# Kernel optimization log

Measured on AMD Instinct MI355X. Metric: run time of the kernel, lower is better.

The kernel has to match this reference:

```python
import jax, jax.numpy as jnp
import numpy as np

B, C, E = 2, 1024, 1024
H = 16            # n_heads as declared (used as per-group feature dim due to module's reshape)
HD = E // H       # 64 — the axis actually batched over in attention


def setup_inputs() -> dict:
    key = jax.random.key(0)
    ks = jax.random.split(key, 5)
    scale = 0.02
    return {
        "x": jax.random.normal(ks[0], (B, C, E), dtype=jnp.float32),
        "W_q": jax.random.normal(ks[1], (E, E), dtype=jnp.float32) * scale,
        "W_k": jax.random.normal(ks[2], (E, E), dtype=jnp.float32) * scale,
        "W_v": jax.random.normal(ks[3], (E, E), dtype=jnp.float32) * scale,
        "W_o": jax.random.normal(ks[4], (E, E), dtype=jnp.float32) * scale,
    }


def reference(x, W_q, W_k, W_v, W_o):
    # nn.Linear: y = x @ W.T  (bias=False)
    def proj_split(W):
        y = jnp.einsum('bce,de->bcd', x, W)              # [B,C,E]
        # view(B, C, HD, H).transpose(1,2) -> [B, HD, C, H]  (faithful to source layout)
        return y.reshape(B, C, HD, H).transpose(0, 2, 1, 3)

    Q = proj_split(W_q)
    K = proj_split(W_k)
    V = proj_split(W_v)

    scale = 1.0 / jnp.sqrt(jnp.asarray(H, dtype=x.dtype))  # sqrt of last dim (= n_heads here)
    scores = jnp.einsum('bdqh,bdkh->bdqk', Q, K) * scale    # [B, HD, C, C]
    weights = jax.nn.softmax(scores, axis=-1)
    out = jnp.einsum('bdqk,bdkh->bdqh', weights, V)         # [B, HD, C, H]
    out = out.transpose(0, 2, 1, 3).reshape(B, C, E)        # [B, C, E]
    out = jnp.einsum('bce,de->bcd', out, W_o)
    return out  # dropout p=0.0 / eval mode: identity
```

## Files before the change

kernel.cpp:

```cpp
#include <hip/hip_runtime.h>
#include <stdint.h>
#include <math.h>


typedef __bf16   bf16x8 __attribute__((ext_vector_type(8)));
typedef float    f32x4  __attribute__((ext_vector_type(4)));

__device__ __forceinline__ unsigned short f2bf(float f) {
    unsigned int u = __float_as_uint(f);
    u += 0x7FFFu + ((u >> 16) & 1u);
    return (unsigned short)(u >> 16);
}

__device__ __forceinline__ unsigned int cvtpk(float lo, float hi) {
    unsigned int r;
    asm("v_cvt_pk_bf16_f32 %0, %1, %2" : "=v"(r) : "v"(lo), "v"(hi));
    return r;
}

__device__ __forceinline__ void gl16(const unsigned short* g, unsigned short* l) {
    __builtin_amdgcn_global_load_lds(
        (const __attribute__((address_space(1))) unsigned int*)g,
        (__attribute__((address_space(3))) unsigned int*)l, 16, 0, 0);
}

__global__ __launch_bounds__(256) void cast_to_bf16(
    const float* __restrict__ x,
    const float* __restrict__ w0, const float* __restrict__ w1,
    const float* __restrict__ w2, const float* __restrict__ w3,
    unsigned short* __restrict__ xb,
    unsigned short* __restrict__ b0, unsigned short* __restrict__ b1,
    unsigned short* __restrict__ b2, unsigned short* __restrict__ b3)
{
    const int z = blockIdx.y;
    const float* src;
    unsigned short* dst;
    size_t off = 0;
    float sc = 1.f;
    if (z < 2)       { src = x;  dst = xb; off = (size_t)z << 20; }
    else if (z == 2) { src = w0; dst = b0; sc = 0.36067376022224085f; }
    else if (z == 3) { src = w1; dst = b1; }
    else if (z == 4) { src = w2; dst = b2; }
    else             { src = w3; dst = b3; }
    const size_t i = off + ((size_t)blockIdx.x * 256 + threadIdx.x) * 4;
    const float4 v = *(const float4*)(src + i);
    *(ushort4*)(dst + i) = make_ushort4(f2bf(v.x * sc), f2bf(v.y * sc),
                                        f2bf(v.z * sc), f2bf(v.w * sc));
}

__global__ __launch_bounds__(256) void gemm128_bt_mfma(
    const unsigned short* __restrict__ A,
    const unsigned short* __restrict__ B0, const unsigned short* __restrict__ B1,
    const unsigned short* __restrict__ B2,
    unsigned short* __restrict__ C0, unsigned short* __restrict__ C1,
    unsigned short* __restrict__ C2,
    int M, int N, int K)
{
    const unsigned short* Bm = (blockIdx.z == 0) ? B0 : (blockIdx.z == 1) ? B1 : B2;
    unsigned short* Cm       = (blockIdx.z == 0) ? C0 : (blockIdx.z == 1) ? C1 : C2;

    __shared__ __align__(16) unsigned short As[2][128 * 32];
    __shared__ __align__(16) unsigned short Bs[2][128 * 32];

    const int t    = threadIdx.x;
    const int lane = t & 63;
    const int w    = t >> 6;
    const int m0   = blockIdx.y * 128;
    const int n0   = blockIdx.x * 128;
    const int wm   = (w & 1) * 64;
    const int wn   = (w >> 1) * 64;

    const int r0 = t >> 2;
    const int c0 = (t & 3) * 8;
    const unsigned short* Apa = A  + (size_t)(m0 + r0) * K + c0;
    const unsigned short* Apb = Apa + (size_t)64 * K;
    const unsigned short* Bpa = Bm + (size_t)(n0 + r0) * K + c0;
    const unsigned short* Bpb = Bpa + (size_t)64 * K;
    unsigned short* lA0 = &As[0][w * 512];
    unsigned short* lA1 = &As[0][2048 + w * 512];
    unsigned short* lB0 = &Bs[0][w * 512];
    unsigned short* lB1 = &Bs[0][2048 + w * 512];
    const int bufStr = 128 * 32;

    f32x4 acc[4][4];
#pragma unroll
    for (int i = 0; i < 4; ++i)
#pragma unroll
        for (int j = 0; j < 4; ++j) acc[i][j] = (f32x4){0.f, 0.f, 0.f, 0.f};

    const int fm = lane & 15;
    const int kg = lane >> 4;

    gl16(Apa, lA0);
    gl16(Apb, lA1);
    gl16(Bpa, lB0);
    gl16(Bpb, lB1);

    int cur = 0;
    for (int k0 = 0; k0 < K; k0 += 32) {
        __syncthreads();

        if (k0 + 32 < K) {
            const int nb = (cur ^ 1);
            gl16(Apa + k0 + 32, lA0 + nb * bufStr);
            gl16(Apb + k0 + 32, lA1 + nb * bufStr);
            gl16(Bpa + k0 + 32, lB0 + nb * bufStr);
            gl16(Bpb + k0 + 32, lB1 + nb * bufStr);
        }

        const unsigned short* Ab = &As[cur][0];
        const unsigned short* Bb = &Bs[cur][0];
        bf16x8 af[4], bfr[4];
#pragma unroll
        for (int im = 0; im < 4; ++im)
            af[im] = *(const bf16x8*)&Ab[(wm + im * 16 + fm) * 32 + kg * 8];
#pragma unroll
        for (int in = 0; in < 4; ++in)
            bfr[in] = *(const bf16x8*)&Bb[(wn + in * 16 + fm) * 32 + kg * 8];
#pragma unroll
        for (int im = 0; im < 4; ++im)
#pragma unroll
            for (int in = 0; in < 4; ++in)
                acc[im][in] = __builtin_amdgcn_mfma_f32_16x16x32_bf16(
                    af[im], bfr[in], acc[im][in], 0, 0, 0);

        cur ^= 1;
    }

#pragma unroll
    for (int im = 0; im < 4; ++im) {
#pragma unroll
        for (int in = 0; in < 4; ++in) {
            const int row = m0 + wm + im * 16 + kg * 4;
            const int col = n0 + wn + in * 16 + fm;
#pragma unroll
            for (int r = 0; r < 4; ++r)
                Cm[(size_t)(row + r) * N + col] = f2bf(acc[im][in][r]);
        }
    }
}

__global__ __launch_bounds__(256) void gemm_bt_mfma(
    const unsigned short* __restrict__ A,
    const unsigned short* __restrict__ B0, const unsigned short* __restrict__ B1,
    const unsigned short* __restrict__ B2,
    void* __restrict__ C0, void* __restrict__ C1, void* __restrict__ C2,
    int M, int N, int K, int bf16out)
{
    const unsigned short* Bm = (blockIdx.z == 0) ? B0 : (blockIdx.z == 1) ? B1 : B2;
    void* Cm                 = (blockIdx.z == 0) ? C0 : (blockIdx.z == 1) ? C1 : C2;

    __shared__ __align__(16) unsigned short As[2][64 * 32];
    __shared__ __align__(16) unsigned short Bs[2][128 * 32];

    const int t    = threadIdx.x;
    const int lane = t & 63;
    const int w    = t >> 6;
    const int m0   = blockIdx.y * 64;
    const int n0   = blockIdx.x * 128;
    const int wm   = (w & 1) * 32;
    const int wn   = (w >> 1) * 64;

    const int r0 = t >> 2;
    const int c0 = (t & 3) * 8;
    const unsigned short* Apa = A  + (size_t)(m0 + r0) * K + c0;
    const unsigned short* Bpa = Bm + (size_t)(n0 + r0) * K + c0;
    const unsigned short* Bpb = Bm + (size_t)(n0 + r0 + 64) * K + c0;
    unsigned short* ldsA  = &As[0][w * 512];
    unsigned short* ldsB0 = &Bs[0][w * 512];
    unsigned short* ldsB1 = &Bs[0][2048 + w * 512];
    const int bufStrA = 64 * 32;
    const int bufStrB = 128 * 32;

    f32x4 acc[2][4];
#pragma unroll
    for (int i = 0; i < 2; ++i)
#pragma unroll
        for (int j = 0; j < 4; ++j) acc[i][j] = (f32x4){0.f, 0.f, 0.f, 0.f};

    const int fm = lane & 15;
    const int kg = lane >> 4;

    gl16(Apa, ldsA);
    gl16(Bpa, ldsB0);
    gl16(Bpb, ldsB1);

    int cur = 0;
    for (int k0 = 0; k0 < K; k0 += 32) {
        __syncthreads();

        if (k0 + 32 < K) {
            const int nb = (cur ^ 1);
            gl16(Apa + k0 + 32, ldsA  + nb * bufStrA);
            gl16(Bpa + k0 + 32, ldsB0 + nb * bufStrB);
            gl16(Bpb + k0 + 32, ldsB1 + nb * bufStrB);
        }

        const unsigned short* Ab = &As[cur][0];
        const unsigned short* Bb = &Bs[cur][0];
        bf16x8 af[2], bfr[4];
#pragma unroll
        for (int im = 0; im < 2; ++im)
            af[im] = *(const bf16x8*)&Ab[(wm + im * 16 + fm) * 32 + kg * 8];
#pragma unroll
        for (int in = 0; in < 4; ++in)
            bfr[in] = *(const bf16x8*)&Bb[(wn + in * 16 + fm) * 32 + kg * 8];
#pragma unroll
        for (int im = 0; im < 2; ++im)
#pragma unroll
            for (int in = 0; in < 4; ++in)
                acc[im][in] = __builtin_amdgcn_mfma_f32_16x16x32_bf16(
                    af[im], bfr[in], acc[im][in], 0, 0, 0);

        cur ^= 1;
    }

#pragma unroll
    for (int im = 0; im < 2; ++im) {
#pragma unroll
        for (int in = 0; in < 4; ++in) {
            const int row = m0 + wm + im * 16 + kg * 4;
            const int col = n0 + wn + in * 16 + fm;
            if (bf16out) {
                unsigned short* cp = (unsigned short*)Cm;
#pragma unroll
                for (int r = 0; r < 4; ++r)
                    cp[(size_t)(row + r) * N + col] = f2bf(acc[im][in][r]);
            } else {
                float* cp = (float*)Cm;
#pragma unroll
                for (int r = 0; r < 4; ++r)
                    cp[(size_t)(row + r) * N + col] = acc[im][in][r];
            }
        }
    }
}

#define VSTRW 40
#define PSTRW 32

__global__ __launch_bounds__(256, 4) void attn_mfma(
    const unsigned short* __restrict__ Qb, const unsigned short* __restrict__ Kb,
    const unsigned short* __restrict__ Vb, unsigned short* __restrict__ Ob)
{
    __shared__ __align__(16) unsigned char smem[37888];

    const int t    = threadIdx.x;
    const int lane = t & 63;
    const int wv   = t >> 6;
    const int fm   = lane & 15;
    const int kg   = lane >> 4;
    const int bh   = blockIdx.y;
    const size_t base = ((size_t)(bh >> 6) << 20) + (size_t)(bh & 63) * 16;
    const int q0 = blockIdx.x * 128;
    const int wk = wv * 32;

    unsigned short* VsT = (unsigned short*)(smem + wv * 1280);
    unsigned short* Ps  = (unsigned short*)(smem + 5120 + wv * 8192);
    float*          Red = (float*)smem;

    union { uint4 u; bf16x8 h; } zz; zz.u = make_uint4(0, 0, 0, 0);
    bf16x8 aq[8];
#pragma unroll
    for (int m = 0; m < 8; ++m) {
        if (kg < 2)
            aq[m] = *(const bf16x8*)(Qb + base +
                     (size_t)(q0 + m * 16 + fm) * 1024 + kg * 8);
        else
            aq[m] = zz.h;
    }

    f32x4 oacc[8];
    float lp[8];
#pragma unroll
    for (int m = 0; m < 8; ++m) {
        oacc[m] = (f32x4){0.f, 0.f, 0.f, 0.f};
        lp[m] = 0.f;
    }

    for (int kt = 0; kt < 1024; kt += 128) {
        {
            const int key = lane >> 1, half = lane & 1;
            const uint4 v = *(const uint4*)(Vb + base +
                             (size_t)(kt + wk + key) * 1024 + half * 8);
            const unsigned short* pv = (const unsigned short*)&v;
#pragma unroll
            for (int d = 0; d < 8; ++d)
                VsT[(half * 8 + d) * VSTRW + key] = pv[d];
        }

        bf16x8 bk0 = zz.h, bk1 = zz.h;
        if (kg < 2) {
            bk0 = *(const bf16x8*)(Kb + base +
                   (size_t)(kt + wk + fm) * 1024 + kg * 8);
            bk1 = *(const bf16x8*)(Kb + base +
                   (size_t)(kt + wk + 16 + fm) * 1024 + kg * 8);
        }

#pragma unroll
        for (int m = 0; m < 8; ++m) {
            f32x4 s0 = __builtin_amdgcn_mfma_f32_16x16x32_bf16(
                bk0, aq[m], (f32x4){0.f, 0.f, 0.f, 0.f}, 0, 0, 0);
            f32x4 s1 = __builtin_amdgcn_mfma_f32_16x16x32_bf16(
                bk1, aq[m], (f32x4){0.f, 0.f, 0.f, 0.f}, 0, 0, 0);
            const float p0 = __builtin_amdgcn_exp2f(s0[0]);
            const float p1 = __builtin_amdgcn_exp2f(s0[1]);
            const float p2 = __builtin_amdgcn_exp2f(s0[2]);
            const float p3 = __builtin_amdgcn_exp2f(s0[3]);
            const float p4 = __builtin_amdgcn_exp2f(s1[0]);
            const float p5 = __builtin_amdgcn_exp2f(s1[1]);
            const float p6 = __builtin_amdgcn_exp2f(s1[2]);
            const float p7 = __builtin_amdgcn_exp2f(s1[3]);
            lp[m] += ((p0 + p1) + (p2 + p3)) + ((p4 + p5) + (p6 + p7));
            unsigned short* prow = Ps + (m * 16 + fm) * PSTRW;
            *(uint2*)&prow[kg * 4]      = make_uint2(cvtpk(p0, p1), cvtpk(p2, p3));
            *(uint2*)&prow[16 + kg * 4] = make_uint2(cvtpk(p4, p5), cvtpk(p6, p7));
        }

        const bf16x8 bv = *(const bf16x8*)&VsT[fm * VSTRW + kg * 8];
#pragma unroll
        for (int m = 0; m < 8; ++m) {
            const bf16x8 ap = *(const bf16x8*)&Ps[(m * 16 + fm) * PSTRW + kg * 8];
            oacc[m] = __builtin_amdgcn_mfma_f32_16x16x32_bf16(ap, bv, oacc[m], 0, 0, 0);
        }
    }

#pragma unroll
    for (int m = 0; m < 8; ++m) {
        lp[m] += __shfl_xor(lp[m], 16, 64);
        lp[m] += __shfl_xor(lp[m], 32, 64);
    }

    __syncthreads();
#pragma unroll
    for (int m = 0; m < 8; ++m) {
#pragma unroll
        for (int r = 0; r < 4; ++r)
            Red[((wv * 128) + m * 16 + kg * 4 + r) * 17 + fm] = oacc[m][r];
        if (kg == 0)
            Red[((wv * 128) + m * 16 + fm) * 17 + 16] = lp[m];
    }
    __syncthreads();

#pragma unroll
    for (int mp = 0; mp < 2; ++mp) {
#pragma unroll
        for (int r = 0; r < 4; ++r) {
            const int q = wv * 32 + mp * 16 + kg * 4 + r;
            const float o = Red[q * 17 + fm]         + Red[(128 + q) * 17 + fm] +
                            Red[(256 + q) * 17 + fm] + Red[(384 + q) * 17 + fm];
            const float l = Red[q * 17 + 16]         + Red[(128 + q) * 17 + 16] +
                            Red[(256 + q) * 17 + 16] + Red[(384 + q) * 17 + 16];
            Ob[base + (size_t)(q0 + q) * 1024 + fm] = f2bf(o / l);
        }
    }
}

extern "C" void kernel_launch(void* const* d_in, const int* in_sizes, int n_in,
                              void* d_out, int out_size, void* d_ws, size_t ws_size,
                              hipStream_t stream) {
    const float* x  = (const float*)d_in[0];
    const float* Wq = (const float*)d_in[1];
    const float* Wk = (const float*)d_in[2];
    const float* Wv = (const float*)d_in[3];
    const float* Wo = (const float*)d_in[4];
    float* out = (float*)d_out;

    const int M = 2048, N = 1024, Kd = 1024;
    const size_t MEG = 1048576;
    unsigned short* ws = (unsigned short*)d_ws;
    unsigned short* xb  = ws;
    unsigned short* Wqb = ws + 2 * MEG;
    unsigned short* Wkb = ws + 3 * MEG;
    unsigned short* Wvb = ws + 4 * MEG;
    unsigned short* Wob = ws + 5 * MEG;
    unsigned short* Qb  = ws + 6 * MEG;
    unsigned short* Kb  = ws + 8 * MEG;
    unsigned short* Vb  = ws + 10 * MEG;
    unsigned short* Ob  = ws + 12 * MEG;

    dim3 gc(1024, 6, 1);
    cast_to_bf16<<<gc, 256, 0, stream>>>(x, Wq, Wk, Wv, Wo, xb, Wqb, Wkb, Wvb, Wob);

    dim3 g1(N / 128, M / 128, 3);
    gemm128_bt_mfma<<<g1, 256, 0, stream>>>(xb, Wqb, Wkb, Wvb, Qb, Kb, Vb, M, N, Kd);

    dim3 g2(8, 128, 1);
    attn_mfma<<<g2, 256, 0, stream>>>(Qb, Kb, Vb, Ob);

    dim3 g3(N / 128, M / 64, 1);
    gemm_bt_mfma<<<g3, 256, 0, stream>>>(Ob, Wob, Wob, Wob, out, out, out, M, N, Kd, 0);
}
```

Baseline: 162.5 us.

## Keep P in registers by permuting V layout, stage K through LDS

Removes the LDS round-trip for the softmax probabilities. P values are packed straight into the MFMA A-operand, and V is stored transposed with a permuted key column order so it matches the register layout of the score accumulator. K is now loaded cooperatively into LDS with coalesced 16-byte loads instead of per-lane global reads. This cuts LDS write/read traffic and shared memory size, but relies on the permutation being correct, and still has no barrier between LDS store and load within each wave.

After: 143.8 us. -11.5%, faster.

```diff
diff --git a/kernel.cpp b/kernel.cpp
--- a/kernel.cpp
+++ b/kernel.cpp
@@ -10,12 +10,6 @@
     unsigned int u = __float_as_uint(f);
     u += 0x7FFFu + ((u >> 16) & 1u);
     return (unsigned short)(u >> 16);
-}
-
-__device__ __forceinline__ unsigned int cvtpk(float lo, float hi) {
-    unsigned int r;
-    asm("v_cvt_pk_bf16_f32 %0, %1, %2" : "=v"(r) : "v"(lo), "v"(hi));
-    return r;
 }
 
 __device__ __forceinline__ void gl16(const unsigned short* g, unsigned short* l) {
@@ -236,14 +230,14 @@
     }
 }
 
-#define VSTRW 40
-#define PSTRW 32
+#define KROWS 40
+#define VROWS 72
 
 __global__ __launch_bounds__(256, 4) void attn_mfma(
     const unsigned short* __restrict__ Qb, const unsigned short* __restrict__ Kb,
     const unsigned short* __restrict__ Vb, unsigned short* __restrict__ Ob)
 {
-    __shared__ __align__(16) unsigned char smem[37888];
+    __shared__ __align__(16) unsigned char smem[34816];
 
     const int t    = threadIdx.x;
     const int lane = t & 63;
@@ -255,9 +249,12 @@
     const int q0 = blockIdx.x * 128;
     const int wk = wv * 32;
 
-    unsigned short* VsT = (unsigned short*)(smem + wv * 1280);
-    unsigned short* Ps  = (unsigned short*)(smem + 5120 + wv * 8192);
+    unsigned short* Ks  = (unsigned short*)(smem + wv * 2560);
+    unsigned short* VsT = (unsigned short*)(smem + 10240 + wv * 2304);
     float*          Red = (float*)smem;
+
+    const int key2 = lane >> 1, half = lane & 1;
+    const int vcol = ((key2 & 15) >> 2) * 8 + (key2 & 3) + ((key2 >> 4) << 2);
 
     union { uint4 u; bf16x8 h; } zz; zz.u = make_uint4(0, 0, 0, 0);
     bf16x8 aq[8];
@@ -280,22 +277,24 @@
 
     for (int kt = 0; kt < 1024; kt += 128) {
         {
-            const int key = lane >> 1, half = lane & 1;
-            const uint4 v = *(const uint4*)(Vb + base +
-                             (size_t)(kt + wk + key) * 1024 + half * 8);
-            const unsigned short* pv = (const unsigned short*)&v;
+            const uint4 kd = *(const uint4*)(Kb + base +
+                              (size_t)(kt + wk + key2) * 1024 + half * 8);
+            *(uint4*)&Ks[key2 * KROWS + half * 8] = kd;
+            const uint4 vd = *(const uint4*)(Vb + base +
+                              (size_t)(kt + wk + key2) * 1024 + half * 8);
+            const unsigned short* pv = (const unsigned short*)&vd;
 #pragma unroll
             for (int d = 0; d < 8; ++d)
-                VsT[(half * 8 + d) * VSTRW + key] = pv[d];
+                VsT[(half * 8 + d) * VROWS + vcol] = pv[d];
         }
 
         bf16x8 bk0 = zz.h, bk1 = zz.h;
         if (kg < 2) {
-            bk0 = *(const bf16x8*)(Kb + base +
-                   (size_t)(kt + wk + fm) * 1024 + kg * 8);
-            bk1 = *(const bf16x8*)(Kb + base +
-                   (size_t)(kt + wk + 16 + fm) * 1024 + kg * 8);
-        }
+            bk0 = *(const bf16x8*)&Ks[fm * KROWS + kg * 8];
+            bk1 = *(const bf16x8*)&Ks[(16 + fm) * KROWS + kg * 8];
+        }
+
+        const bf16x8 bv = *(const bf16x8*)&VsT[fm * VROWS + kg * 8];
 
 #pragma unroll
         for (int m = 0; m < 8; ++m) {
@@ -312,16 +311,13 @@
             const float p6 = __builtin_amdgcn_exp2f(s1[2]);
             const float p7 = __builtin_amdgcn_exp2f(s1[3]);
             lp[m] += ((p0 + p1) + (p2 + p3)) + ((p4 + p5) + (p6 + p7));
-            unsigned short* prow = Ps + (m * 16 + fm) * PSTRW;
-            *(uint2*)&prow[kg * 4]      = make_uint2(cvtpk(p0, p1), cvtpk(p2, p3));
-            *(uint2*)&prow[16 + kg * 4] = make_uint2(cvtpk(p4, p5), cvtpk(p6, p7));
-        }
-
-        const bf16x8 bv = *(const bf16x8*)&VsT[fm * VSTRW + kg * 8];
-#pragma unroll
-        for (int m = 0; m < 8; ++m) {
-            const bf16x8 ap = *(const bf16x8*)&Ps[(m * 16 + fm) * PSTRW + kg * 8];
-            oacc[m] = __builtin_amdgcn_mfma_f32_16x16x32_bf16(ap, bv, oacc[m], 0, 0, 0);
+            bf16x8 aph;
+            aph[0] = (__bf16)p0; aph[1] = (__bf16)p1;
+            aph[2] = (__bf16)p2; aph[3] = (__bf16)p3;
+            aph[4] = (__bf16)p4; aph[5] = (__bf16)p5;
+            aph[6] = (__bf16)p6; aph[7] = (__bf16)p7;
+            oacc[m] = __builtin_amdgcn_mfma_f32_16x16x32_bf16(
+                aph, bv, oacc[m], 0, 0, 0);
         }
     }
 
```
